# Kernel optimization log

Measured on AMD Instinct MI355X. Metric: run time of the kernel, lower is better.

## Reference

```python
import jax, jax.numpy as jnp
import numpy as np

IN, H, F2, OUT, B = 257, 400, 600, 257, 16384


def setup_inputs() -> dict:
    key = jax.random.key(0)
    ks = jax.random.split(key, 32)
    n = lambda i, shape, s: jax.random.normal(ks[i], shape, jnp.float32) * s
    d = {
        "x": n(0, (IN, B), 1.0),
        "h1": n(1, (H, B), 1.0),
        "h2": n(2, (H, B), 1.0),
        # fc1: 257 -> 400
        "W_fc1": n(3, (H, IN), 0.05),
        "b_fc1": n(4, (H,), 0.05),
        # GRU layer 1 (hidden 400)
        "Wiz1": n(5, (H, H), 0.05), "Wir1": n(6, (H, H), 0.05), "Win1": n(7, (H, H), 0.05),
        "Whz1": n(8, (H, H), 0.05), "Whr1": n(9, (H, H), 0.05), "Whn1": n(10, (H, H), 0.05),
        "biz1": n(11, (H,), 0.05), "bir1": n(12, (H,), 0.05), "bin1": n(13, (H,), 0.05),
        "bhz1": n(14, (H,), 0.05), "bhr1": n(15, (H,), 0.05), "bhn1": n(16, (H,), 0.05),
        # GRU layer 2
        "Wiz2": n(17, (H, H), 0.05), "Wir2": n(18, (H, H), 0.05), "Win2": n(19, (H, H), 0.05),
        "Whz2": n(20, (H, H), 0.05), "Whr2": n(21, (H, H), 0.05), "Whn2": n(22, (H, H), 0.05),
        "biz2": n(23, (H,), 0.05), "bir2": n(24, (H,), 0.05), "bin2": n(25, (H,), 0.05),
        "bhz2": n(26, (H,), 0.05), "bhr2": n(27, (H,), 0.05), "bhn2": n(28, (H,), 0.05),
        # fc2: 400 -> 600, fc3: 600 -> 600, fc4: 600 -> 257
        "W_fc2": n(29, (F2, H), 0.05), "b_fc2": n(30, (F2,), 0.05),
        "W_fc3": n(31, (F2, F2), 0.05), "b_fc3": jnp.zeros((F2,), jnp.float32),
        "W_fc4": jax.random.normal(jax.random.fold_in(key, 100), (OUT, F2), jnp.float32) * 0.05,
        "b_fc4": jnp.zeros((OUT,), jnp.float32),
    }
    return d


def _gru_cell(xin, h, Wiz, Wir, Win, Whz, Whr, Whn, biz, bir, bin_, bhz, bhr, bhn):
    # xin: [H, B], h: [H, B]; column-vector convention W @ x, matching the source.
    r = jax.nn.sigmoid(Wir @ xin + bir[:, None] + Whr @ h + bhr[:, None])
    z = jax.nn.sigmoid(Wiz @ xin + biz[:, None] + Whz @ h + bhz[:, None])
    n_ = jnp.tanh(Win @ xin + bin_[:, None] + r * (Whn @ h + bhn[:, None]))
    return (1.0 - z) * n_ + z * h


def reference(x, h1, h2, W_fc1, b_fc1,
              Wiz1, Wir1, Win1, Whz1, Whr1, Whn1,
              biz1, bir1, bin1, bhz1, bhr1, bhn1,
              Wiz2, Wir2, Win2, Whz2, Whr2, Whn2,
              biz2, bir2, bin2, bhz2, bhr2, bhn2,
              W_fc2, b_fc2, W_fc3, b_fc3, W_fc4, b_fc4):
    fc1 = W_fc1 @ x + b_fc1[:, None]                       # [400, B]
    h1n = _gru_cell(fc1, h1, Wiz1, Wir1, Win1, Whz1, Whr1, Whn1,
                    biz1, bir1, bin1, bhz1, bhr1, bhn1)    # [400, B]
    h2n = _gru_cell(h1n, h2, Wiz2, Wir2, Win2, Whz2, Whr2, Whn2,
                    biz2, bir2, bin2, bhz2, bhr2, bhn2)    # [400, B]
    y = jax.nn.relu(W_fc2 @ h2n + b_fc2[:, None])          # [600, B]
    y = jax.nn.relu(W_fc3 @ y + b_fc3[:, None])            # [600, B]
    return jax.nn.sigmoid(W_fc4 @ y + b_fc4[:, None])      # [257, B]
```

## Files before the change

kernel.cpp:

```cpp
#include <hip/hip_runtime.h>
#include <math.h>


#define B_TOTAL 16384
#define H16_TOTAL 3452928L
#define PREP_TOTAL 3460352L

typedef _Float16 h8 __attribute__((ext_vector_type(8)));
typedef float f4 __attribute__((ext_vector_type(4)));

#define GLL(g, l) __builtin_amdgcn_global_load_lds(                         \
    (const __attribute__((address_space(1))) void*)(g),                     \
    (__attribute__((address_space(3))) void*)(l), 16, 0, 0)

#define MFMA(d, a_, b_) d = __builtin_amdgcn_mfma_f32_16x16x32_f16(a_, b_, d, 0, 0, 0)

__device__ inline int swzg(int row, int c) { return row * 8 + (c ^ (row & 7)); }

__device__ inline void swz_bt_mt(int bid, int& bt, int& mt) {
  const int xcd = bid & 7;
  const int i = bid >> 3;
  bt = xcd * 16 + (i & 15);
  mt = i >> 4;
}

__constant__ int kJsrc[32] = {3, 5,6,7, 8,9,10, 17,18,19, 20,21,22, 29, 31, 33,
                              4, 11,12,13, 14,15,16, 23,24,25, 26,27,28, 30, 32, 34};
__constant__ int kJM[32]   = {400, 400,400,400, 400,400,400, 400,400,400, 400,400,400, 600, 600, 257,
                              400, 400,400,400, 400,400,400, 400,400,400, 400,400,400, 600, 600, 257};
__constant__ int kJK[32]   = {257, 400,400,400, 400,400,400, 400,400,400, 400,400,400, 400, 600, 600,
                              1,1,1,1, 1,1,1, 1,1,1, 1,1,1, 1, 1, 1};
__constant__ int kJKp[32]  = {320, 448,448,448, 448,448,448, 448,448,448, 448,448,448, 448, 640, 640,
                              1,1,1,1, 1,1,1, 1,1,1, 1,1,1, 1, 1, 1};
__constant__ long kJcum[33] = {0,143360,344064,544768,745472,946176,1146880,1347584,1548288,1748992,
  1949696,2150400,2351104,2551808,2838528,3248128,3452928,3453376,3453824,3454272,3454720,3455168,
  3455616,3456064,3456512,3456960,3457408,3457856,3458304,3458752,3459392,3460032,3460352};

struct SrcPtrs { const float* p[35]; };

__global__ __launch_bounds__(256) void prep_weights(SrcPtrs sp, _Float16* __restrict__ w16,
                                                    float* __restrict__ b32) {
  long w = (long)blockIdx.x * 256 + threadIdx.x;
  if (w >= PREP_TOTAL) return;
  int j = 0;
  #pragma unroll 1
  while (j < 31 && kJcum[j + 1] <= w) j++;
  long local = w - kJcum[j];
  int Kp = kJKp[j];
  int m = (int)(local / Kp);
  int k = (int)(local - (long)m * Kp);
  float v = 0.f;
  if (m < kJM[j] && k < kJK[j]) v = sp.p[kJsrc[j]][(long)m * kJK[j] + k];
  if (j < 16) w16[w] = (_Float16)v;
  else        b32[w - H16_TOTAL] = v;
}

__global__ __launch_bounds__(256) void transpose_in(const float* __restrict__ x,
                                                    const float* __restrict__ h1,
                                                    const float* __restrict__ h2,
                                                    _Float16* __restrict__ dx,
                                                    _Float16* __restrict__ dh1,
                                                    _Float16* __restrict__ dh2) {
  __shared__ float t[32][33];
  int b = blockIdx.x;
  const float* src; _Float16* dst; int F, nFT;
  if (b < 5120)        { src = x;  dst = dx;  F = 257; nFT = 10; }
  else if (b < 12288)  { b -= 5120;  src = h1; dst = dh1; F = 400; nFT = 14; }
  else                 { b -= 12288; src = h2; dst = dh2; F = 400; nFT = 14; }
  const int Fp = nFT * 32;
  const int ft = b % nFT;
  const int bt = b / nFT;
  const int ci = threadIdx.x & 31, ri = threadIdx.x >> 5;
  #pragma unroll
  for (int p = 0; p < 4; ++p) {
    int f = ft * 32 + ri + p * 8;
    float v = (f < F) ? src[(long)f * B_TOTAL + bt * 32 + ci] : 0.f;
    t[ri + p * 8][ci] = v;
  }
  __syncthreads();
  #pragma unroll
  for (int p = 0; p < 4; ++p) {
    int bb = bt * 32 + ri + p * 8;
    dst[(long)bb * Fp + ft * 32 + ci] = (_Float16)t[ci][ri + p * 8];
  }
}

__global__ __launch_bounds__(256) void transpose_out(const float* __restrict__ src,
                                                     float* __restrict__ dst) {
  __shared__ float t[32][33];
  const int nFT = 10;
  const int ft = blockIdx.x % nFT;
  const int bt = blockIdx.x / nFT;
  const int ci = threadIdx.x & 31, ri = threadIdx.x >> 5;
  #pragma unroll
  for (int p = 0; p < 4; ++p)
    t[ri + p * 8][ci] = src[(long)(bt * 32 + ri + p * 8) * 320 + ft * 32 + ci];
  __syncthreads();
  #pragma unroll
  for (int p = 0; p < 4; ++p) {
    int f = ft * 32 + ri + p * 8;
    if (f < 257) dst[(long)f * B_TOTAL + bt * 32 + ci] = t[ci][ri + p * 8];
  }
}

template <int ACT, int OUTF32, int K, int M>
__global__ __launch_bounds__(512, 6) void gemm_tn(const _Float16* __restrict__ A,
                                                  const _Float16* __restrict__ W,
                                                  const float* __restrict__ bias,
                                                  void* __restrict__ C) {
  constexpr int KT = K / 64;
  __shared__ __align__(16) _Float16 As2[2][128 * 64];
  __shared__ __align__(16) _Float16 Ws2[2][64 * 64];
  const int tid = threadIdx.x;
  const int l = tid & 63;
  const int w = tid >> 6;
  int bt, mt;
  swz_bt_mt(blockIdx.x, bt, mt);
  const int wr = w >> 1, wc = w & 1;
  const int sc = ((l & 7) ^ (l >> 3)) * 8;
  const int srow = tid >> 3;

  const _Float16* ag = A + (long)(bt * 128 + srow) * K + sc;
  const _Float16* wg = W + (long)(mt * 64 + srow) * K + sc;

  f4 acc[2][2];
  #pragma unroll
  for (int i = 0; i < 2; ++i)
    #pragma unroll
    for (int jj = 0; jj < 2; ++jj) acc[i][jj] = (f4){0.f, 0.f, 0.f, 0.f};

  const int lg = l >> 4;
  const int arow = wr * 32 + (l & 15);
  const int wrow = wc * 32 + (l & 15);

  auto stage = [&](int b, int t) {
    GLL(ag + t * 64, (char*)As2[b] + w * 1024);
    GLL(ag + t * 64 + (long)64 * K, (char*)As2[b] + w * 1024 + 8192);
    GLL(wg + t * 64, (char*)Ws2[b] + w * 1024);
  };

  stage(0, 0);
  __syncthreads();
  #pragma unroll
  for (int i = 0; i < KT; ++i) {
    if (i + 1 < KT) stage((i + 1) & 1, i + 1);
    const h8* AsV = (const h8*)As2[i & 1];
    const h8* WsV = (const h8*)Ws2[i & 1];
    h8 b00 = WsV[swzg(wrow, lg)],      b01 = WsV[swzg(wrow, 4 | lg)];
    h8 b10 = WsV[swzg(wrow + 16, lg)], b11 = WsV[swzg(wrow + 16, 4 | lg)];
    #pragma unroll
    for (int fm = 0; fm < 2; ++fm) {
      h8 a0 = AsV[swzg(arow + fm * 16, lg)];
      h8 a1 = AsV[swzg(arow + fm * 16, 4 | lg)];
      MFMA(acc[fm][0], a0, b00); MFMA(acc[fm][0], a1, b01);
      MFMA(acc[fm][1], a0, b10); MFMA(acc[fm][1], a1, b11);
    }
    __syncthreads();
  }

  const int jloc = wc * 32 + (l & 15);
  const int colBase = mt * 64 + jloc;
  if (OUTF32) {
    const int rowBase = bt * 128 + wr * 32 + (l >> 4) * 4;
    #pragma unroll
    for (int fn = 0; fn < 2; ++fn) {
      const float bb = bias[colBase + fn * 16];
      #pragma unroll
      for (int fm = 0; fm < 2; ++fm)
        #pragma unroll
        for (int r = 0; r < 4; ++r) {
          float x = acc[fm][fn][r] + bb;
          if (ACT == 2) x = 1.f / (1.f + __expf(-x));
          ((float*)C)[(long)(rowBase + fm * 16 + r) * M + colBase + fn * 16] = x;
        }
    }
  } else {
    _Float16* scr = (_Float16*)As2;
    const int rowLoc = wr * 32 + (l >> 4) * 4;
    #pragma unroll
    for (int fn = 0; fn < 2; ++fn) {
      const float bb = bias[colBase + fn * 16];
      #pragma unroll
      for (int fm = 0; fm < 2; ++fm)
        #pragma unroll
        for (int r = 0; r < 4; ++r) {
          float x = acc[fm][fn][r] + bb;
          if (ACT == 1) x = fmaxf(x, 0.f);
          scr[(rowLoc + fm * 16 + r) * 72 + jloc + fn * 16] = (_Float16)x;
        }
    }
    __syncthreads();
    const int rrow = tid >> 2, rq = tid & 3;
    h8 v0 = *(const h8*)(scr + rrow * 72 + rq * 16);
    h8 v1 = *(const h8*)(scr + rrow * 72 + rq * 16 + 8);
    _Float16* gp = (_Float16*)C + (long)(bt * 128 + rrow) * M + mt * 64 + rq * 16;
    *(h8*)gp = v0;
    *(h8*)(gp + 8) = v1;
  }
}

__global__ __launch_bounds__(512, 4) void gemm_gru(const _Float16* __restrict__ Ax,
                                                   const _Float16* __restrict__ Ah,
                                                   const _Float16* __restrict__ Wi_,
                                                   const _Float16* __restrict__ Wh_,
                                                   const float* __restrict__ bi,
                                                   const float* __restrict__ bh,
                                                   _Float16* __restrict__ Hn) {
  __shared__ __align__(16) _Float16 As2[2][128 * 64];
  __shared__ __align__(16) _Float16 Ws2[2][3][64 * 64];
  const int tid = threadIdx.x;
  const int l = tid & 63;
  const int w = tid >> 6;
  int bt, mt;
  swz_bt_mt(blockIdx.x, bt, mt);
  const int wr = w >> 1, wc = w & 1;
  const int sc = ((l & 7) ^ (l >> 3)) * 8;
  const int srow = tid >> 3;

  const long arowg = (long)(bt * 128 + srow) * 448 + sc;
  const long wrowg = (long)(mt * 64 + srow) * 448 + sc;

  f4 acc[4][2][2];
  #pragma unroll
  for (int g = 0; g < 4; ++g)
    #pragma unroll
    for (int i = 0; i < 2; ++i)
      #pragma unroll
      for (int jj = 0; jj < 2; ++jj) acc[g][i][jj] = (f4){0.f, 0.f, 0.f, 0.f};

  const int lg = l >> 4;
  const int arow = wr * 32 + (l & 15);
  const int wrow = wc * 32 + (l & 15);

  auto stage = [&](int b, int i) {
    const _Float16* ab = (i >= 7) ? Ah : Ax;
    const _Float16* wb = (i >= 7) ? Wh_ : Wi_;
    const int kc = ((i >= 7) ? (mt + i - 6) % 7 : i) * 64;
    GLL(ab + arowg + kc, (char*)As2[b] + w * 1024);
    GLL(ab + arowg + kc + 64 * 448, (char*)As2[b] + w * 1024 + 8192);
    #pragma unroll
    for (int g = 0; g < 3; ++g)
      GLL(wb + wrowg + (long)g * 200704 + kc, (char*)Ws2[b][g] + w * 1024);
  };

  stage(0, 0);
  __syncthreads();
  #pragma unroll
  for (int i = 0; i < 14; ++i) {
    if (i < 13) stage((i + 1) & 1, i + 1);
    const h8* AsV = (const h8*)As2[i & 1];
    const h8* WsV = (const h8*)Ws2[i & 1][0];
    h8 a00 = AsV[swzg(arow, lg)],      a01 = AsV[swzg(arow, 4 | lg)];
    h8 a10 = AsV[swzg(arow + 16, lg)], a11 = AsV[swzg(arow + 16, 4 | lg)];
    #pragma unroll
    for (int g = 0; g < 3; ++g) {
      const int d = (g == 2) ? ((i < 7) ? 2 : 3) : g;
      h8 b00 = WsV[g * 512 + swzg(wrow, lg)];
      h8 b01 = WsV[g * 512 + swzg(wrow, 4 | lg)];
      h8 b10 = WsV[g * 512 + swzg(wrow + 16, lg)];
      h8 b11 = WsV[g * 512 + swzg(wrow + 16, 4 | lg)];
      MFMA(acc[d][0][0], a00, b00); MFMA(acc[d][0][0], a01, b01);
      MFMA(acc[d][0][1], a00, b10); MFMA(acc[d][0][1], a01, b11);
      MFMA(acc[d][1][0], a10, b00); MFMA(acc[d][1][0], a11, b01);
      MFMA(acc[d][1][1], a10, b10); MFMA(acc[d][1][1], a11, b11);
    }
    __syncthreads();
  }

  const _Float16* Alast = As2[1];
  _Float16* scr = (_Float16*)Ws2;
  const int jloc = wc * 32 + (l & 15);
  const int rowLoc = wr * 32 + (l >> 4) * 4;
  #pragma unroll
  for (int fn = 0; fn < 2; ++fn) {
    const int j = mt * 64 + jloc + fn * 16;
    const float bz = bi[j] + bh[j];
    const float br = bi[448 + j] + bh[448 + j];
    const float bnx = bi[896 + j], bnh = bh[896 + j];
    #pragma unroll
    for (int fm = 0; fm < 2; ++fm) {
      #pragma unroll
      for (int r = 0; r < 4; ++r) {
        const float zz = 1.f / (1.f + __expf(-(acc[0][fm][fn][r] + bz)));
        const float rr = 1.f / (1.f + __expf(-(acc[1][fm][fn][r] + br)));
        const float nn = (acc[2][fm][fn][r] + bnx) + rr * (acc[3][fm][fn][r] + bnh);
        const float th = 1.f - 2.f / (__expf(2.f * nn) + 1.f);
        const int row = rowLoc + fm * 16 + r;
        const int col = jloc + fn * 16;
        const float ho = (float)Alast[swzg(row, col >> 3) * 8 + (col & 7)];
        scr[row * 72 + col] = (_Float16)((1.f - zz) * th + zz * ho);
      }
    }
  }
  __syncthreads();
  const int rrow = tid >> 2, rq = tid & 3;
  h8 v0 = *(const h8*)(scr + rrow * 72 + rq * 16);
  h8 v1 = *(const h8*)(scr + rrow * 72 + rq * 16 + 8);
  _Float16* gp = Hn + (long)(bt * 128 + rrow) * 448 + mt * 64 + rq * 16;
  *(h8*)gp = v0;
  *(h8*)(gp + 8) = v1;
}

extern "C" void kernel_launch(void* const* d_in, const int* in_sizes, int n_in,
                              void* d_out, int out_size, void* d_ws, size_t ws_size,
                              hipStream_t stream) {
  char* ws = (char*)d_ws;
  _Float16* W16  = (_Float16*)(ws);
  float*    BIAS = (float*)(ws + 6905856L);
  _Float16* buf2 = (_Float16*)(ws + 6935552L);
  _Float16* buf3 = (_Float16*)(ws + 27907072L);
  _Float16* buf4 = (_Float16*)(ws + 48878592L);
  _Float16* buf5 = (_Float16*)(ws + 63558656L);
  _Float16* buf6 = (_Float16*)(ws + 78238720L);
  float* outT = (float*)buf2;
  if (ws_size < 92918784UL) return;

  SrcPtrs sp;
  for (int i = 0; i < 35; ++i) sp.p[i] = (const float*)d_in[i];

  prep_weights<<<dim3(13517), dim3(256), 0, stream>>>(sp, W16, BIAS);
  transpose_in<<<dim3(19456), dim3(256), 0, stream>>>((const float*)d_in[0], (const float*)d_in[1],
                                                      (const float*)d_in[2], buf2, buf4, buf5);

  gemm_tn<0, 0, 320, 448><<<dim3(128 * 7), dim3(512), 0, stream>>>(buf2, W16, BIAS, (void*)buf3);
  gemm_gru<<<dim3(128 * 7), dim3(512), 0, stream>>>(buf3, buf4, W16 + 143360, W16 + 745472,
                                                    BIAS + 448, BIAS + 1792, buf6);
  gemm_gru<<<dim3(128 * 7), dim3(512), 0, stream>>>(buf6, buf5, W16 + 1347584, W16 + 1949696,
                                                    BIAS + 3136, BIAS + 4480, buf4);
  gemm_tn<1, 0, 448, 640><<<dim3(128 * 10), dim3(512), 0, stream>>>(buf4, W16 + 2551808, BIAS + 5824, (void*)buf2);
  gemm_tn<1, 0, 640, 640><<<dim3(128 * 10), dim3(512), 0, stream>>>(buf2, W16 + 2838528, BIAS + 6464, (void*)buf3);
  gemm_tn<2, 1, 640, 320><<<dim3(128 * 5), dim3(512), 0, stream>>>(buf3, W16 + 3248128, BIAS + 7104, (void*)outT);

  transpose_out<<<dim3(10 * 512), dim3(256), 0, stream>>>(outT, (float*)d_out);
}
```

Measured before the change: 395.0 us.

## Double gemm_tn batch tile to 256 rows and use explicit vmcnt waits

```diff
diff --git a/kernel.cpp b/kernel.cpp
--- a/kernel.cpp
+++ b/kernel.cpp
@@ -14,6 +14,10 @@
     (__attribute__((address_space(3))) void*)(l), 16, 0, 0)
 
 #define MFMA(d, a_, b_) d = __builtin_amdgcn_mfma_f32_16x16x32_f16(a_, b_, d, 0, 0, 0)
+#define WAITV5() asm volatile("s_waitcnt vmcnt(5)" ::: "memory")
+#define WAITV0() asm volatile("s_waitcnt vmcnt(0)" ::: "memory")
+#define WAITL0() asm volatile("s_waitcnt lgkmcnt(0)" ::: "memory")
+#define BAR()    __builtin_amdgcn_s_barrier()
 
 __device__ inline int swzg(int row, int c) { return row * 8 + (c ^ (row & 7)); }
 
@@ -22,6 +26,12 @@
   const int i = bid >> 3;
   bt = xcd * 16 + (i & 15);
   mt = i >> 4;
+}
+__device__ inline void swz64(int bid, int& bt, int& mt) {
+  const int xcd = bid & 7;
+  const int i = bid >> 3;
+  bt = xcd * 8 + (i & 7);
+  mt = i >> 3;
 }
 
 __constant__ int kJsrc[32] = {3, 5,6,7, 8,9,10, 17,18,19, 20,21,22, 29, 31, 33,
@@ -104,69 +114,74 @@
 }
 
 template <int ACT, int OUTF32, int K, int M>
-__global__ __launch_bounds__(512, 6) void gemm_tn(const _Float16* __restrict__ A,
+__global__ __launch_bounds__(512, 4) void gemm_tn(const _Float16* __restrict__ A,
                                                   const _Float16* __restrict__ W,
                                                   const float* __restrict__ bias,
                                                   void* __restrict__ C) {
   constexpr int KT = K / 64;
-  __shared__ __align__(16) _Float16 As2[2][128 * 64];
+  __shared__ __align__(16) _Float16 As2[2][256 * 64];
   __shared__ __align__(16) _Float16 Ws2[2][64 * 64];
   const int tid = threadIdx.x;
   const int l = tid & 63;
   const int w = tid >> 6;
   int bt, mt;
-  swz_bt_mt(blockIdx.x, bt, mt);
+  swz64(blockIdx.x, bt, mt);
   const int wr = w >> 1, wc = w & 1;
   const int sc = ((l & 7) ^ (l >> 3)) * 8;
   const int srow = tid >> 3;
 
-  const _Float16* ag = A + (long)(bt * 128 + srow) * K + sc;
+  const _Float16* ag = A + (long)(bt * 256 + srow) * K + sc;
   const _Float16* wg = W + (long)(mt * 64 + srow) * K + sc;
 
-  f4 acc[2][2];
-  #pragma unroll
-  for (int i = 0; i < 2; ++i)
+  f4 acc[4][2];
+  #pragma unroll
+  for (int i = 0; i < 4; ++i)
     #pragma unroll
     for (int jj = 0; jj < 2; ++jj) acc[i][jj] = (f4){0.f, 0.f, 0.f, 0.f};
 
   const int lg = l >> 4;
-  const int arow = wr * 32 + (l & 15);
+  const int arow = wr * 64 + (l & 15);
   const int wrow = wc * 32 + (l & 15);
 
   auto stage = [&](int b, int t) {
-    GLL(ag + t * 64, (char*)As2[b] + w * 1024);
-    GLL(ag + t * 64 + (long)64 * K, (char*)As2[b] + w * 1024 + 8192);
+    #pragma unroll
+    for (int j = 0; j < 4; ++j)
+      GLL(ag + t * 64 + (long)j * 64 * K, (char*)As2[b] + j * 8192 + w * 1024);
     GLL(wg + t * 64, (char*)Ws2[b] + w * 1024);
   };
 
   stage(0, 0);
-  __syncthreads();
+  WAITV0();
+  BAR();
   #pragma unroll
   for (int i = 0; i < KT; ++i) {
-    if (i + 1 < KT) stage((i + 1) & 1, i + 1);
+    if (i + 1 < KT) { stage((i + 1) & 1, i + 1); WAITV5(); }
+    else            { WAITV0(); }
+    BAR();
     const h8* AsV = (const h8*)As2[i & 1];
     const h8* WsV = (const h8*)Ws2[i & 1];
     h8 b00 = WsV[swzg(wrow, lg)],      b01 = WsV[swzg(wrow, 4 | lg)];
     h8 b10 = WsV[swzg(wrow + 16, lg)], b11 = WsV[swzg(wrow + 16, 4 | lg)];
     #pragma unroll
-    for (int fm = 0; fm < 2; ++fm) {
+    for (int fm = 0; fm < 4; ++fm) {
       h8 a0 = AsV[swzg(arow + fm * 16, lg)];
       h8 a1 = AsV[swzg(arow + fm * 16, 4 | lg)];
       MFMA(acc[fm][0], a0, b00); MFMA(acc[fm][0], a1, b01);
       MFMA(acc[fm][1], a0, b10); MFMA(acc[fm][1], a1, b11);
     }
-    __syncthreads();
+    WAITL0();
+    BAR();
   }
 
   const int jloc = wc * 32 + (l & 15);
   const int colBase = mt * 64 + jloc;
   if (OUTF32) {
-    const int rowBase = bt * 128 + wr * 32 + (l >> 4) * 4;
+    const int rowBase = bt * 256 + wr * 64 + (l >> 4) * 4;
     #pragma unroll
     for (int fn = 0; fn < 2; ++fn) {
       const float bb = bias[colBase + fn * 16];
       #pragma unroll
-      for (int fm = 0; fm < 2; ++fm)
+      for (int fm = 0; fm < 4; ++fm)
         #pragma unroll
         for (int r = 0; r < 4; ++r) {
           float x = acc[fm][fn][r] + bb;
@@ -176,26 +191,30 @@
     }
   } else {
     _Float16* scr = (_Float16*)As2;
-    const int rowLoc = wr * 32 + (l >> 4) * 4;
+    const int rowLoc = wr * 64 + (l >> 4) * 4;
     #pragma unroll
     for (int fn = 0; fn < 2; ++fn) {
       const float bb = bias[colBase + fn * 16];
       #pragma unroll
-      for (int fm = 0; fm < 2; ++fm)
+      for (int fm = 0; fm < 4; ++fm)
         #pragma unroll
         for (int r = 0; r < 4; ++r) {
           float x = acc[fm][fn][r] + bb;
           if (ACT == 1) x = fmaxf(x, 0.f);
-          scr[(rowLoc + fm * 16 + r) * 72 + jloc + fn * 16] = (_Float16)x;
+          scr[(rowLoc + fm * 16 + r) * 80 + jloc + fn * 16] = (_Float16)x;
         }
     }
     __syncthreads();
-    const int rrow = tid >> 2, rq = tid & 3;
-    h8 v0 = *(const h8*)(scr + rrow * 72 + rq * 16);
-    h8 v1 = *(const h8*)(scr + rrow * 72 + rq * 16 + 8);
-    _Float16* gp = (_Float16*)C + (long)(bt * 128 + rrow) * M + mt * 64 + rq * 16;
-    *(h8*)gp = v0;
-    *(h8*)(gp + 8) = v1;
+    const int rq = tid & 3;
+    #pragma unroll
+    for (int p = 0; p < 2; ++p) {
+      const int rrow = p * 128 + (tid >> 2);
+      h8 v0 = *(const h8*)(scr + rrow * 80 + rq * 16);
+      h8 v1 = *(const h8*)(scr + rrow * 80 + rq * 16 + 8);
+      _Float16* gp = (_Float16*)C + (long)(bt * 256 + rrow) * M + mt * 64 + rq * 16;
+      *(h8*)gp = v0;
+      *(h8*)(gp + 8) = v1;
+    }
   }
 }
 
@@ -244,10 +263,13 @@
   };
 
   stage(0, 0);
-  __syncthreads();
+  WAITV0();
+  BAR();
   #pragma unroll
   for (int i = 0; i < 14; ++i) {
-    if (i < 13) stage((i + 1) & 1, i + 1);
+    if (i < 13) { stage((i + 1) & 1, i + 1); WAITV5(); }
+    else        { WAITV0(); }
+    BAR();
     const h8* AsV = (const h8*)As2[i & 1];
     const h8* WsV = (const h8*)Ws2[i & 1][0];
     h8 a00 = AsV[swzg(arow, lg)],      a01 = AsV[swzg(arow, 4 | lg)];
@@ -264,7 +286,8 @@
       MFMA(acc[d][1][0], a10, b00); MFMA(acc[d][1][0], a11, b01);
       MFMA(acc[d][1][1], a10, b10); MFMA(acc[d][1][1], a11, b11);
     }
-    __syncthreads();
+    WAITL0();
+    BAR();
   }
 
   const _Float16* Alast = As2[1];
@@ -288,14 +311,14 @@
         const int row = rowLoc + fm * 16 + r;
         const int col = jloc + fn * 16;
         const float ho = (float)Alast[swzg(row, col >> 3) * 8 + (col & 7)];
-        scr[row * 72 + col] = (_Float16)((1.f - zz) * th + zz * ho);
+        scr[row * 80 + col] = (_Float16)((1.f - zz) * th + zz * ho);
       }
     }
   }
   __syncthreads();
   const int rrow = tid >> 2, rq = tid & 3;
-  h8 v0 = *(const h8*)(scr + rrow * 72 + rq * 16);
-  h8 v1 = *(const h8*)(scr + rrow * 72 + rq * 16 + 8);
+  h8 v0 = *(const h8*)(scr + rrow * 80 + rq * 16);
+  h8 v1 = *(const h8*)(scr + rrow * 80 + rq * 16 + 8);
   _Float16* gp = Hn + (long)(bt * 128 + rrow) * 448 + mt * 64 + rq * 16;
   *(h8*)gp = v0;
   *(h8*)(gp + 8) = v1;
@@ -322,14 +345,14 @@
   transpose_in<<<dim3(19456), dim3(256), 0, stream>>>((const float*)d_in[0], (const float*)d_in[1],
                                                       (const float*)d_in[2], buf2, buf4, buf5);
 
-  gemm_tn<0, 0, 320, 448><<<dim3(128 * 7), dim3(512), 0, stream>>>(buf2, W16, BIAS, (void*)buf3);
+  gemm_tn<0, 0, 320, 448><<<dim3(64 * 7), dim3(512), 0, stream>>>(buf2, W16, BIAS, (void*)buf3);
   gemm_gru<<<dim3(128 * 7), dim3(512), 0, stream>>>(buf3, buf4, W16 + 143360, W16 + 745472,
                                                     BIAS + 448, BIAS + 1792, buf6);
   gemm_gru<<<dim3(128 * 7), dim3(512), 0, stream>>>(buf6, buf5, W16 + 1347584, W16 + 1949696,
                                                     BIAS + 3136, BIAS + 4480, buf4);
-  gemm_tn<1, 0, 448, 640><<<dim3(128 * 10), dim3(512), 0, stream>>>(buf4, W16 + 2551808, BIAS + 5824, (void*)buf2);
-  gemm_tn<1, 0, 640, 640><<<dim3(128 * 10), dim3(512), 0, stream>>>(buf2, W16 + 2838528, BIAS + 6464, (void*)buf3);
-  gemm_tn<2, 1, 640, 320><<<dim3(128 * 5), dim3(512), 0, stream>>>(buf3, W16 + 3248128, BIAS + 7104, (void*)outT);
+  gemm_tn<1, 0, 448, 640><<<dim3(64 * 10), dim3(512), 0, stream>>>(buf4, W16 + 2551808, BIAS + 5824, (void*)buf2);
+  gemm_tn<1, 0, 640, 640><<<dim3(64 * 10), dim3(512), 0, stream>>>(buf2, W16 + 2838528, BIAS + 6464, (void*)buf3);
+  gemm_tn<2, 1, 640, 320><<<dim3(64 * 5), dim3(512), 0, stream>>>(buf3, W16 + 3248128, BIAS + 7104, (void*)outT);
 
   transpose_out<<<dim3(10 * 512), dim3(256), 0, stream>>>(outT, (float*)d_out);
 }
```

Measured after the change: 403.4 us. 1.02x slower.
